# Optimization experiments

Measured on AMD Instinct MI355X. Metric: run time of the kernel, lower is better.

Reference implementation:

```python
import jax, jax.numpy as jnp
import numpy as np

BLOCK = 64  # NF4 block size
SCALING = 32.0 / 16.0  # lora_alpha / r

# Standard NF4 (normal-float 4-bit) codebook, 16 levels
NF4_TABLE = jnp.asarray([
    -1.0, -0.6961928009986877, -0.5250730514526367, -0.39491748809814453,
    -0.28444138169288635, -0.18477343022823334, -0.09105003625154495, 0.0,
    0.07958029955625534, 0.16093020141124725, 0.24611230194568634,
    0.33791524171829224, 0.44070982933044434, 0.5626170039176941,
    0.7229568362236023, 1.0], dtype=jnp.float32)


def dequant_nf4(codes, scales):
    # codes: [out, in] int in [0,16); scales: [out, in//BLOCK] float
    out_f, in_f = codes.shape
    w = NF4_TABLE[codes].reshape(out_f, in_f // BLOCK, BLOCK)
    w = w * scales[:, :, None]
    return w.reshape(out_f, in_f)


def setup_inputs() -> dict:
    key = jax.random.key(0)
    k1, k2, k3, k4, k5 = jax.random.split(key, 5)
    B, S, D_in, D_out, R = 4, 2048, 4096, 4096, 16
    x = jax.random.normal(k1, (B, S, D_in), dtype=jnp.float32)
    codes = jax.random.randint(k2, (D_out, D_in), 0, 16, dtype=jnp.int32)
    scales = jax.random.uniform(k3, (D_out, D_in // BLOCK), dtype=jnp.float32)
    lora_A = jax.random.normal(k4, (R, D_in), dtype=jnp.float32) * (1.0 / np.sqrt(D_in))
    lora_B = jax.random.normal(k5, (D_out, R), dtype=jnp.float32) * 0.02
    return {"x": x, "codes": codes, "scales": scales,
            "lora_A": lora_A, "lora_B": lora_B}


def reference(x, codes, scales, lora_A, lora_B):
    # Base path: F.linear(x, dequant(W))  -> x @ W^T
    W = dequant_nf4(codes, scales)            # [out, in]
    base = jnp.einsum('bsd,od->bso', x, W)    # [B, S, out]
    # LoRA path (dropout p=0.0 -> identity): (x @ A^T) @ B^T * scaling
    lora = jnp.einsum('bsr,or->bso', jnp.einsum('bsd,rd->bsr', x, lora_A), lora_B)
    return base + lora * SCALING
```

## Files before the change

kernel.cpp:

```cpp
#include <hip/hip_runtime.h>
#include <hip/hip_bf16.h>

typedef __attribute__((ext_vector_type(8))) short short8;
typedef __attribute__((ext_vector_type(4))) short short4v;
typedef __attribute__((ext_vector_type(4))) float floatx4;

#define M_DIM 8192
#define N_DIM 4096
#define K_DIM 4096
#define BM 128
#define BN 128
#define BK 64

__device__ __constant__ float NF4_TAB[16] = {
    -1.0f, -0.6961928009986877f, -0.5250730514526367f, -0.39491748809814453f,
    -0.28444138169288635f, -0.18477343022823334f, -0.09105003625154495f, 0.0f,
    0.07958029955625534f, 0.16093020141124725f, 0.24611230194568634f,
    0.33791524171829224f, 0.44070982933044434f, 0.5626170039176941f,
    0.7229568362236023f, 1.0f};

__global__ __launch_bounds__(256)
void dequant_lora_kernel(const int* __restrict__ codes,
                         const float* __restrict__ scales,
                         const float* __restrict__ la,
                         const float* __restrict__ lb,
                         short4v* __restrict__ W) {
    __shared__ float tab[16];
    if (threadIdx.x < 16) tab[threadIdx.x] = NF4_TAB[threadIdx.x];
    __syncthreads();

    const int kb = blockIdx.x & 3;
    const int n0 = (blockIdx.x >> 2) << 4;
    const int k0 = kb * 1024 + threadIdx.x * 4;

    float4 a[16];
#pragma unroll
    for (int r = 0; r < 16; r++)
        a[r] = *(const float4*)(la + (size_t)r * K_DIM + k0);

#pragma unroll 4
    for (int i = 0; i < 16; i++) {
        const int n = n0 + i;
        int4 c = *(const int4*)(codes + (size_t)n * K_DIM + k0);
        float s = scales[(n << 6) + (k0 >> 6)];
        const float* bp = lb + (n << 4);
        float acc0 = 0.f, acc1 = 0.f, acc2 = 0.f, acc3 = 0.f;
#pragma unroll
        for (int r = 0; r < 16; r++) {
            float br = bp[r];
            acc0 += br * a[r].x;
            acc1 += br * a[r].y;
            acc2 += br * a[r].z;
            acc3 += br * a[r].w;
        }
        union { short4v v; __hip_bfloat16 h[4]; } u;
        u.h[0] = __float2bfloat16(tab[c.x] * s + 2.0f * acc0);
        u.h[1] = __float2bfloat16(tab[c.y] * s + 2.0f * acc1);
        u.h[2] = __float2bfloat16(tab[c.z] * s + 2.0f * acc2);
        u.h[3] = __float2bfloat16(tab[c.w] * s + 2.0f * acc3);
        W[((size_t)n * K_DIM + k0) >> 2] = u.v;
    }
}

__global__ void cast_x_kernel(const float* __restrict__ x,
                              short8* __restrict__ xb) {
    int g = blockIdx.x * blockDim.x + threadIdx.x;
    const float4* xp = (const float4*)(x + (size_t)g * 8);
    float4 v0 = xp[0], v1 = xp[1];
    union { short8 v; __hip_bfloat16 h[8]; } u;
    u.h[0] = __float2bfloat16(v0.x);
    u.h[1] = __float2bfloat16(v0.y);
    u.h[2] = __float2bfloat16(v0.z);
    u.h[3] = __float2bfloat16(v0.w);
    u.h[4] = __float2bfloat16(v1.x);
    u.h[5] = __float2bfloat16(v1.y);
    u.h[6] = __float2bfloat16(v1.z);
    u.h[7] = __float2bfloat16(v1.w);
    xb[g] = u.v;
}

#define GL2LDS(gsrc, ldst)                                                   \
    __builtin_amdgcn_global_load_lds(                                        \
        (const __attribute__((address_space(1))) void*)(gsrc),               \
        (__attribute__((address_space(3))) void*)(ldst), 16, 0, 0)

__global__ __launch_bounds__(256, 3)
void gemm_bt_kernel(const __hip_bfloat16* __restrict__ A,
                    const __hip_bfloat16* __restrict__ B,
                    float* __restrict__ C) {
    __shared__ __align__(16) __hip_bfloat16 sA[BM * BK];
    __shared__ __align__(16) __hip_bfloat16 sB[BN * BK];
    const int tid = threadIdx.x;
    const int wave = tid >> 6;
    const int lane = tid & 63;
    const int q = lane >> 4;
    const int t = lane & 15;
    const int wm = wave >> 1;
    const int wn = wave & 1;
    const int bm0 = blockIdx.y * BM;
    const int bn0 = blockIdx.x * BN;

    floatx4 acc[4][4] = {};

    const __hip_bfloat16* ga[4];
    const __hip_bfloat16* gb[4];
#pragma unroll
    for (int i = 0; i < 4; i++) {
        int rt = i * 32 + (tid >> 3);
        int cb = (tid & 7) ^ (rt & 7);
        ga[i] = A + (size_t)(bm0 + rt) * K_DIM + cb * 8;
        gb[i] = B + (size_t)(bn0 + rt) * K_DIM + cb * 8;
    }

    for (int k0 = 0; k0 < K_DIM; k0 += BK) {
#pragma unroll
        for (int i = 0; i < 4; i++) {
            GL2LDS(ga[i] + k0, (char*)sA + (i * 256 + wave * 64) * 16);
            GL2LDS(gb[i] + k0, (char*)sB + (i * 256 + wave * 64) * 16);
        }
        __syncthreads();
#pragma unroll
        for (int ks = 0; ks < BK; ks += 32) {
            short8 af[4], bfr[4];
#pragma unroll
            for (int mi = 0; mi < 4; mi++) {
                int row = wm * 64 + mi * 16 + t;
                int cb = (ks >> 3) + q;
                af[mi] = *(const short8*)&sA[row * 64 + ((cb ^ (row & 7)) << 3)];
            }
#pragma unroll
            for (int ni = 0; ni < 4; ni++) {
                int row = wn * 64 + ni * 16 + t;
                int cb = (ks >> 3) + q;
                bfr[ni] = *(const short8*)&sB[row * 64 + ((cb ^ (row & 7)) << 3)];
            }
#pragma unroll
            for (int mi = 0; mi < 4; mi++)
#pragma unroll
                for (int ni = 0; ni < 4; ni++)
                    acc[mi][ni] = __builtin_amdgcn_mfma_f32_16x16x32_bf16(
                        af[mi], bfr[ni], acc[mi][ni], 0, 0, 0);
        }
        __syncthreads();
    }

#pragma unroll
    for (int mi = 0; mi < 4; mi++) {
        int row0 = bm0 + wm * 64 + mi * 16 + q * 4;
#pragma unroll
        for (int ni = 0; ni < 4; ni++) {
            int col = bn0 + wn * 64 + ni * 16 + t;
            float* cp = C + (size_t)row0 * N_DIM + col;
#pragma unroll
            for (int r = 0; r < 4; r++) cp[(size_t)r * N_DIM] = acc[mi][ni][r];
        }
    }
}

extern "C" void kernel_launch(void* const* d_in, const int* in_sizes, int n_in,
                              void* d_out, int out_size, void* d_ws,
                              size_t ws_size, hipStream_t stream) {
    const float* x = (const float*)d_in[0];
    const int* codes = (const int*)d_in[1];
    const float* scales = (const float*)d_in[2];
    const float* loraA = (const float*)d_in[3];
    const float* loraB = (const float*)d_in[4];
    float* out = (float*)d_out;

    char* ws = (char*)d_ws;
    __hip_bfloat16* xb = (__hip_bfloat16*)ws;
    __hip_bfloat16* Wb = (__hip_bfloat16*)(ws + 67108864);

    dequant_lora_kernel<<<dim3(4 * (N_DIM / 16)), dim3(256), 0, stream>>>(
        codes, scales, loraA, loraB, (short4v*)Wb);
    cast_x_kernel<<<dim3((M_DIM * (K_DIM / 8)) / 256), dim3(256), 0, stream>>>(
        x, (short8*)xb);
    gemm_bt_kernel<<<dim3(N_DIM / BN, M_DIM / BM), dim3(256), 0, stream>>>(
        xb, Wb, out);
}
```

Before: 514.9 us.

## Merge prep kernels and switch GEMM to 32x32x16 MFMA tiles

Fuses the dequant+LoRA kernel and the x-to-bf16 cast into one launch, with each dequant block now handling 4 output rows instead of 16 so there are more blocks. The GEMM inner loop moves from 16x16x32 MFMA on a 4x4 grid of tiles to 32x32x16 MFMA on a 2x2 grid per wave. The larger MFMA is meant to raise compute throughput and cut LDS fragment reads, and the fused launch removes one kernel boundary. In exchange the output store pattern changes, and the more numerous dequant blocks reload the LoRA A vectors more often.

```diff
diff --git a/kernel.cpp b/kernel.cpp
--- a/kernel.cpp
+++ b/kernel.cpp
@@ -3,7 +3,7 @@
 
 typedef __attribute__((ext_vector_type(8))) short short8;
 typedef __attribute__((ext_vector_type(4))) short short4v;
-typedef __attribute__((ext_vector_type(4))) float floatx4;
+typedef __attribute__((ext_vector_type(16))) float floatx16;
 
 #define M_DIM 8192
 #define N_DIM 4096
@@ -11,6 +11,9 @@
 #define BM 128
 #define BN 128
 #define BK 64
+
+#define CAST_BLOCKS 16384
+#define DEQ_BLOCKS 4096
 
 __device__ __constant__ float NF4_TAB[16] = {
     -1.0f, -0.6961928009986877f, -0.5250730514526367f, -0.39491748809814453f,
@@ -20,17 +23,32 @@
     0.7229568362236023f, 1.0f};
 
 __global__ __launch_bounds__(256)
-void dequant_lora_kernel(const int* __restrict__ codes,
-                         const float* __restrict__ scales,
-                         const float* __restrict__ la,
-                         const float* __restrict__ lb,
-                         short4v* __restrict__ W) {
+void prep_kernel(const float* __restrict__ x, const int* __restrict__ codes,
+                 const float* __restrict__ scales, const float* __restrict__ la,
+                 const float* __restrict__ lb, short8* __restrict__ xb,
+                 short4v* __restrict__ W) {
+    if (blockIdx.x >= DEQ_BLOCKS) {
+        int g = (blockIdx.x - DEQ_BLOCKS) * blockDim.x + threadIdx.x;
+        const float4* xp = (const float4*)(x + (size_t)g * 8);
+        float4 v0 = xp[0], v1 = xp[1];
+        union { short8 v; __hip_bfloat16 h[8]; } u;
+        u.h[0] = __float2bfloat16(v0.x);
+        u.h[1] = __float2bfloat16(v0.y);
+        u.h[2] = __float2bfloat16(v0.z);
+        u.h[3] = __float2bfloat16(v0.w);
+        u.h[4] = __float2bfloat16(v1.x);
+        u.h[5] = __float2bfloat16(v1.y);
+        u.h[6] = __float2bfloat16(v1.z);
+        u.h[7] = __float2bfloat16(v1.w);
+        xb[g] = u.v;
+        return;
+    }
     __shared__ float tab[16];
     if (threadIdx.x < 16) tab[threadIdx.x] = NF4_TAB[threadIdx.x];
     __syncthreads();
 
     const int kb = blockIdx.x & 3;
-    const int n0 = (blockIdx.x >> 2) << 4;
+    const int n0 = (blockIdx.x >> 2) << 2;
     const int k0 = kb * 1024 + threadIdx.x * 4;
 
     float4 a[16];
@@ -38,8 +56,8 @@
     for (int r = 0; r < 16; r++)
         a[r] = *(const float4*)(la + (size_t)r * K_DIM + k0);
 
-#pragma unroll 4
-    for (int i = 0; i < 16; i++) {
+#pragma unroll
+    for (int i = 0; i < 4; i++) {
         const int n = n0 + i;
         int4 c = *(const int4*)(codes + (size_t)n * K_DIM + k0);
         float s = scales[(n << 6) + (k0 >> 6)];
@@ -62,23 +80,6 @@
     }
 }
 
-__global__ void cast_x_kernel(const float* __restrict__ x,
-                              short8* __restrict__ xb) {
-    int g = blockIdx.x * blockDim.x + threadIdx.x;
-    const float4* xp = (const float4*)(x + (size_t)g * 8);
-    float4 v0 = xp[0], v1 = xp[1];
-    union { short8 v; __hip_bfloat16 h[8]; } u;
-    u.h[0] = __float2bfloat16(v0.x);
-    u.h[1] = __float2bfloat16(v0.y);
-    u.h[2] = __float2bfloat16(v0.z);
-    u.h[3] = __float2bfloat16(v0.w);
-    u.h[4] = __float2bfloat16(v1.x);
-    u.h[5] = __float2bfloat16(v1.y);
-    u.h[6] = __float2bfloat16(v1.z);
-    u.h[7] = __float2bfloat16(v1.w);
-    xb[g] = u.v;
-}
-
 #define GL2LDS(gsrc, ldst)                                                   \
     __builtin_amdgcn_global_load_lds(                                        \
         (const __attribute__((address_space(1))) void*)(gsrc),               \
@@ -93,14 +94,14 @@
     const int tid = threadIdx.x;
     const int wave = tid >> 6;
     const int lane = tid & 63;
-    const int q = lane >> 4;
-    const int t = lane & 15;
+    const int l31 = lane & 31;
+    const int half = lane >> 5;
     const int wm = wave >> 1;
     const int wn = wave & 1;
     const int bm0 = blockIdx.y * BM;
     const int bn0 = blockIdx.x * BN;
 
-    floatx4 acc[4][4] = {};
+    floatx16 acc[2][2] = {};
 
     const __hip_bfloat16* ga[4];
     const __hip_bfloat16* gb[4];
@@ -120,39 +121,40 @@
         }
         __syncthreads();
 #pragma unroll
-        for (int ks = 0; ks < BK; ks += 32) {
-            short8 af[4], bfr[4];
+        for (int ks = 0; ks < BK; ks += 16) {
+            short8 af[2], bfr[2];
+            const int cb = (ks >> 3) + half;
 #pragma unroll
-            for (int mi = 0; mi < 4; mi++) {
-                int row = wm * 64 + mi * 16 + t;
-                int cb = (ks >> 3) + q;
+            for (int mi = 0; mi < 2; mi++) {
+                int row = wm * 64 + mi * 32 + l31;
                 af[mi] = *(const short8*)&sA[row * 64 + ((cb ^ (row & 7)) << 3)];
             }
 #pragma unroll
-            for (int ni = 0; ni < 4; ni++) {
-                int row = wn * 64 + ni * 16 + t;
-                int cb = (ks >> 3) + q;
+            for (int ni = 0; ni < 2; ni++) {
+                int row = wn * 64 + ni * 32 + l31;
                 bfr[ni] = *(const short8*)&sB[row * 64 + ((cb ^ (row & 7)) << 3)];
             }
 #pragma unroll
-            for (int mi = 0; mi < 4; mi++)
+            for (int mi = 0; mi < 2; mi++)
 #pragma unroll
-                for (int ni = 0; ni < 4; ni++)
-                    acc[mi][ni] = __builtin_amdgcn_mfma_f32_16x16x32_bf16(
+                for (int ni = 0; ni < 2; ni++)
+                    acc[mi][ni] = __builtin_amdgcn_mfma_f32_32x32x16_bf16(
                         af[mi], bfr[ni], acc[mi][ni], 0, 0, 0);
         }
         __syncthreads();
     }
 
 #pragma unroll
-    for (int mi = 0; mi < 4; mi++) {
-        int row0 = bm0 + wm * 64 + mi * 16 + q * 4;
+    for (int mi = 0; mi < 2; mi++) {
+        int rbase = bm0 + wm * 64 + mi * 32 + 4 * half;
 #pragma unroll
-        for (int ni = 0; ni < 4; ni++) {
-            int col = bn0 + wn * 64 + ni * 16 + t;
-            float* cp = C + (size_t)row0 * N_DIM + col;
+        for (int ni = 0; ni < 2; ni++) {
+            int col = bn0 + wn * 64 + ni * 32 + l31;
 #pragma unroll
-            for (int r = 0; r < 4; r++) cp[(size_t)r * N_DIM] = acc[mi][ni][r];
+            for (int reg = 0; reg < 16; reg++) {
+                int row = rbase + (reg & 3) + 8 * (reg >> 2);
+                C[(size_t)row * N_DIM + col] = acc[mi][ni][reg];
+            }
         }
     }
 }
@@ -171,10 +173,8 @@
     __hip_bfloat16* xb = (__hip_bfloat16*)ws;
     __hip_bfloat16* Wb = (__hip_bfloat16*)(ws + 67108864);
 
-    dequant_lora_kernel<<<dim3(4 * (N_DIM / 16)), dim3(256), 0, stream>>>(
-        codes, scales, loraA, loraB, (short4v*)Wb);
-    cast_x_kernel<<<dim3((M_DIM * (K_DIM / 8)) / 256), dim3(256), 0, stream>>>(
-        x, (short8*)xb);
+    prep_kernel<<<dim3(DEQ_BLOCKS + CAST_BLOCKS), dim3(256), 0, stream>>>(
+        x, codes, scales, loraA, loraB, (short8*)xb, (short4v*)Wb);
     gemm_bt_kernel<<<dim3(N_DIM / BN, M_DIM / BM), dim3(256), 0, stream>>>(
         xb, Wb, out);
 }
```

Measured after the change: 539.0 us. 4.7% more time.
